# Kernel optimization log

Measured on AMD Instinct MI355X. Metric: run time of the kernel, lower is better.

The kernel has to match this reference:

```python
import jax, jax.numpy as jnp
import numpy as np

B, S, H, D = 2, 2048, 32, 128
DM = H * D  # 4096
SCALE = D ** -0.5


def setup_inputs() -> dict:
    key = jax.random.key(0)
    ks = jax.random.split(key, 7)
    std = DM ** -0.5
    return {
        "q": jax.random.normal(ks[0], (B, S, DM), dtype=jnp.float32),
        "k": jax.random.normal(ks[1], (B, S, DM), dtype=jnp.float32),
        "v": jax.random.normal(ks[2], (B, S, DM), dtype=jnp.float32),
        # torch nn.Linear weights are [out_features, in_features]
        "Wq": jax.random.normal(ks[3], (DM, DM), dtype=jnp.float32) * std,
        "Wk": jax.random.normal(ks[4], (DM, DM), dtype=jnp.float32) * std,
        "Wv": jax.random.normal(ks[5], (DM, DM), dtype=jnp.float32) * std,
        "Wo": jax.random.normal(ks[6], (DM, DM), dtype=jnp.float32) * std,
    }


def reference(q, k, v, Wq, Wk, Wv, Wo):
    # Linear: y = x @ W^T (no bias, qkv_bias=False)
    qp = q @ Wq.T  # [B,S,DM]
    kp = k @ Wk.T
    vp = v @ Wv.T
    # [B,S,DM] -> [B,H,S,D]
    qh = qp.reshape(B, S, H, D).transpose(0, 2, 1, 3)
    kh = kp.reshape(B, S, H, D).transpose(0, 2, 1, 3)
    vh = vp.reshape(B, S, H, D).transpose(0, 2, 1, 3)
    # scaled dot-product attention (no mask; attn_mask default None)
    scores = jnp.einsum("bhqd,bhkd->bhqk", qh, kh) * SCALE  # [B,H,S,S]
    probs = jax.nn.softmax(scores, axis=-1)
    ctx = jnp.einsum("bhqk,bhkd->bhqd", probs, vh)  # [B,H,S,D]
    ctx = ctx.transpose(0, 2, 1, 3).reshape(B, S, DM)
    return ctx @ Wo.T  # [B,S,DM]
```

## Files before the change

### kernel.cpp

```cpp
#include <hip/hip_runtime.h>
#include <hip/hip_bf16.h>
#include <stdint.h>


using u16 = unsigned short;
using u32 = unsigned int;

typedef __attribute__((ext_vector_type(8))) short bf16x8;
typedef __attribute__((ext_vector_type(8))) u16 u16x8;
typedef __attribute__((ext_vector_type(4))) float f32x4;

#define MFMA_BF16(A, B, C) __builtin_amdgcn_mfma_f32_16x16x32_bf16((A), (B), (C), 0, 0, 0)

static constexpr int kS = 2048, kDM = 4096, kD = 128;
static constexpr size_t kMat = (size_t)4096 * 4096;
static constexpr float kScaleLog2e = 0.08838834764831845f * 1.44269504088896340736f;

static __device__ __forceinline__ void gload_lds16(const u16* g, u16* l) {
  __builtin_amdgcn_global_load_lds((const __attribute__((address_space(1))) void*)g,
                                   (__attribute__((address_space(3))) void*)l, 16, 0, 0);
}

static __device__ __forceinline__ u16 f2bf(float f) {
  u32 u = __float_as_uint(f);
  u32 r = u + 0x7FFFu + ((u >> 16) & 1u);
  return (u16)(r >> 16);
}

static __device__ __forceinline__ float bf2f(u16 x) {
  return __uint_as_float((u32)x << 16);
}

static __device__ __forceinline__ u16 nbf(float f) {
  union { __hip_bfloat16 h; u16 u; } cv;
  cv.h = __float2bfloat16(f);
  return cv.u;
}

static __device__ __forceinline__ u16x8 cvt8(float4 a, float4 b) {
  u16x8 r;
  r[0] = f2bf(a.x); r[1] = f2bf(a.y); r[2] = f2bf(a.z); r[3] = f2bf(a.w);
  r[4] = f2bf(b.x); r[5] = f2bf(b.y); r[6] = f2bf(b.z); r[7] = f2bf(b.w);
  return r;
}

__global__ __launch_bounds__(256) void cvt_kernel(
    const float* __restrict__ s0, const float* __restrict__ s1,
    const float* __restrict__ s2, const float* __restrict__ s3,
    const float* __restrict__ s4, const float* __restrict__ s5,
    const float* __restrict__ s6, u16* __restrict__ dst) {
  const int y = blockIdx.y;
  const float* s = (y == 0) ? s0 : (y == 1) ? s1 : (y == 2) ? s2 : (y == 3) ? s3
                  : (y == 4) ? s4 : (y == 5) ? s5 : s6;
  u16* d = dst + (size_t)y * kMat;
  const size_t nchunk = kMat / 8;
  const size_t step = (size_t)gridDim.x * 256;
  for (size_t c = (size_t)blockIdx.x * 256 + threadIdx.x; c < nchunk; c += step) {
    const float* p = s + c * 8;
    float4 a = *(const float4*)p;
    float4 b = *(const float4*)(p + 4);
    *(u16x8*)(d + c * 8) = cvt8(a, b);
  }
}

template <bool TRANS, bool OUT_F32>
static __device__ __forceinline__ void gemm256(const u16* __restrict__ X,
                                               const u16* __restrict__ W,
                                               void* __restrict__ Yv,
                                               u16* __restrict__ lds) {
  constexpr int NT = kDM / 64;
  const int tid = threadIdx.x;
  const int lane = tid & 63;
  const int w = tid >> 6;
  const int fr = lane & 15;
  const int fq = lane >> 4;
  const int wr = w >> 2;
  const int wc = w & 3;
  const int m0 = blockIdx.y * 256;
  const int n0 = blockIdx.x * 256;

  const int srow = tid >> 3;
  const int scol = ((tid & 7) ^ (srow & 7)) * 8;
  const u16* Xrow = X + (size_t)(m0 + srow) * kDM + scol;
  const u16* Wrow = W + (size_t)(n0 + srow) * kDM + scol;
  const int w512 = w * 512;

  const int rBb = wc * 64 + fr;
  const int rAb = wr * 128 + fr;
  const int swz = fr & 7;

  f32x4 acc[8][4] = {};

#define STAGE2(ROWP, qrow, k0, ldq)                                       \
  do {                                                                    \
    gload_lds16((ROWP) + (size_t)(qrow) * kDM + (k0), &lds[(ldq) + w512]); \
    gload_lds16((ROWP) + (size_t)((qrow) + 64) * kDM + (k0),              \
                &lds[(ldq) + 4096 + w512]);                               \
  } while (0)

  STAGE2(Wrow, 0, 0, 0);
  STAGE2(Wrow, 128, 0, 8192);
  STAGE2(Xrow, 0, 0, 16384);
  STAGE2(Xrow, 128, 0, 24576);
  STAGE2(Wrow, 0, 64, 32768);
  STAGE2(Wrow, 128, 64, 32768 + 8192);
  STAGE2(Xrow, 0, 64, 32768 + 16384);
  asm volatile("s_waitcnt vmcnt(6)" ::: "memory");
  __builtin_amdgcn_s_barrier();

  for (int t = 0; t < NT; ++t) {
    const int d = t & 1;
    const int Boff = d * 32768;
    const int Aoff = Boff + 16384;
    bf16x8 bfr[4][2], af[8][2];

#pragma unroll
    for (int nf = 0; nf < 4; ++nf)
#pragma unroll
      for (int ks = 0; ks < 2; ++ks)
        bfr[nf][ks] = *(const bf16x8*)&lds[Boff + (rBb + nf * 16) * 64 +
                                           (((ks * 4 + fq) ^ swz) * 8)];
#pragma unroll
    for (int mi = 0; mi < 4; ++mi)
#pragma unroll
      for (int ks = 0; ks < 2; ++ks)
        af[mi][ks] = *(const bf16x8*)&lds[Aoff + (rAb + mi * 16) * 64 +
                                          (((ks * 4 + fq) ^ swz) * 8)];
    if (t + 1 < NT) STAGE2(Xrow, 128, (t + 1) * 64, ((t + 1) & 1) * 32768 + 24576);
    __builtin_amdgcn_s_barrier();
    __builtin_amdgcn_s_setprio(1);
#pragma unroll
    for (int mi = 0; mi < 2; ++mi)
#pragma unroll
      for (int nf = 0; nf < 4; ++nf)
#pragma unroll
        for (int ks = 0; ks < 2; ++ks)
          acc[mi][nf] = TRANS ? MFMA_BF16(bfr[nf][ks], af[mi][ks], acc[mi][nf])
                              : MFMA_BF16(af[mi][ks], bfr[nf][ks], acc[mi][nf]);
    __builtin_amdgcn_s_setprio(0);
    __builtin_amdgcn_s_barrier();

#pragma unroll
    for (int mi = 4; mi < 6; ++mi)
#pragma unroll
      for (int ks = 0; ks < 2; ++ks)
        af[mi][ks] = *(const bf16x8*)&lds[Aoff + (rAb + mi * 16) * 64 +
                                          (((ks * 4 + fq) ^ swz) * 8)];
    if (t + 2 < NT) STAGE2(Wrow, 0, (t + 2) * 64, d * 32768 + 0);
    __builtin_amdgcn_s_barrier();
    __builtin_amdgcn_s_setprio(1);
#pragma unroll
    for (int mi = 2; mi < 4; ++mi)
#pragma unroll
      for (int nf = 0; nf < 4; ++nf)
#pragma unroll
        for (int ks = 0; ks < 2; ++ks)
          acc[mi][nf] = TRANS ? MFMA_BF16(bfr[nf][ks], af[mi][ks], acc[mi][nf])
                              : MFMA_BF16(af[mi][ks], bfr[nf][ks], acc[mi][nf]);
    __builtin_amdgcn_s_setprio(0);
    __builtin_amdgcn_s_barrier();

#pragma unroll
    for (int mi = 6; mi < 8; ++mi)
#pragma unroll
      for (int ks = 0; ks < 2; ++ks)
        af[mi][ks] = *(const bf16x8*)&lds[Aoff + (rAb + mi * 16) * 64 +
                                          (((ks * 4 + fq) ^ swz) * 8)];
    if (t + 2 < NT) STAGE2(Wrow, 128, (t + 2) * 64, d * 32768 + 8192);
    __builtin_amdgcn_s_barrier();
    __builtin_amdgcn_s_setprio(1);
#pragma unroll
    for (int mi = 4; mi < 6; ++mi)
#pragma unroll
      for (int nf = 0; nf < 4; ++nf)
#pragma unroll
        for (int ks = 0; ks < 2; ++ks)
          acc[mi][nf] = TRANS ? MFMA_BF16(bfr[nf][ks], af[mi][ks], acc[mi][nf])
                              : MFMA_BF16(af[mi][ks], bfr[nf][ks], acc[mi][nf]);
    __builtin_amdgcn_s_setprio(0);
    asm volatile("s_waitcnt lgkmcnt(0)" ::: "memory");
    __builtin_amdgcn_s_barrier();

    if (t + 2 < NT) STAGE2(Xrow, 0, (t + 2) * 64, d * 32768 + 16384);
    __builtin_amdgcn_s_barrier();
    __builtin_amdgcn_s_setprio(1);
#pragma unroll
    for (int mi = 6; mi < 8; ++mi)
#pragma unroll
      for (int nf = 0; nf < 4; ++nf)
#pragma unroll
        for (int ks = 0; ks < 2; ++ks)
          acc[mi][nf] = TRANS ? MFMA_BF16(bfr[nf][ks], af[mi][ks], acc[mi][nf])
                              : MFMA_BF16(af[mi][ks], bfr[nf][ks], acc[mi][nf]);
    __builtin_amdgcn_s_setprio(0);
    if (t + 2 < NT)
      asm volatile("s_waitcnt vmcnt(6)" ::: "memory");
    else
      asm volatile("s_waitcnt vmcnt(0)" ::: "memory");
    __builtin_amdgcn_s_barrier();
  }
#undef STAGE2

#pragma unroll
  for (int mi = 0; mi < 8; ++mi)
#pragma unroll
    for (int nf = 0; nf < 4; ++nf) {
      int row, col;
      if constexpr (TRANS) {
        row = n0 + wc * 64 + nf * 16 + fq * 4;
        col = m0 + wr * 128 + mi * 16 + fr;
      } else {
        row = m0 + wr * 128 + mi * 16 + fq * 4;
        col = n0 + wc * 64 + nf * 16 + fr;
      }
      if constexpr (OUT_F32) {
        float* yp = (float*)Yv + (size_t)row * kDM + col;
#pragma unroll
        for (int i = 0; i < 4; ++i) yp[(size_t)i * kDM] = acc[mi][nf][i];
      } else {
        u16* yp = (u16*)Yv + (size_t)row * kDM + col;
#pragma unroll
        for (int i = 0; i < 4; ++i) yp[(size_t)i * kDM] = f2bf(acc[mi][nf][i]);
      }
    }
}

__global__ __launch_bounds__(512, 2) void proj_qk256_kernel(const u16* __restrict__ wsb,
                                                            u16* __restrict__ qp,
                                                            u16* __restrict__ kp) {
  __shared__ u16 lds[65536];
  const int z = blockIdx.z;
  gemm256<false, false>(wsb + (size_t)z * kMat, wsb + (size_t)(3 + z) * kMat,
                        z ? kp : qp, lds);
}

__global__ __launch_bounds__(512, 2) void proj_vT256_kernel(const u16* __restrict__ wsb,
                                                            u16* __restrict__ vpT) {
  __shared__ u16 lds[65536];
  gemm256<true, false>(wsb + 2 * kMat, wsb + 5 * kMat, vpT, lds);
}

__global__ __launch_bounds__(512, 2) void out_proj256_kernel(const u16* __restrict__ ctx,
                                                             const u16* __restrict__ Wob,
                                                             float* __restrict__ out) {
  __shared__ u16 lds[65536];
  gemm256<false, true>(ctx, Wob, out, lds);
}

template <bool A_BF16, bool TRANS, bool OUT_F32>
static __device__ __forceinline__ void gemm_conv(const void* Xv, const float* Wf,
                                                 void* Yv, u16* __restrict__ Als,
                                                 u16* __restrict__ Bls) {
  constexpr int KD = 4096;
  const int tid = threadIdx.x;
  const int lane = tid & 63;
  const int w = tid >> 6;
  const int fr = lane & 15;
  const int fq = lane >> 4;
  const int m0 = blockIdx.y * 128;
  const int n0 = blockIdx.x * 128;

  const int r0 = tid >> 2, cc0 = (tid & 3) * 8;
  const int r1 = r0 + 64;
  const int sr = lane >> 2, sc = (lane & 3) * 8;
  const int u0 = w * 2, u1 = w * 2 + 1;

  const u16* Xb = (const u16*)Xv;
  const float* Xf = (const float*)Xv;

  const int wm = (w >> 1) * 64;
  const int wn = (w & 1) * 64;

  f32x4 acc[4][4] = {};

  for (int kt = 0; kt < KD / 32; ++kt) {
    const int ko = kt * 32;
    if constexpr (A_BF16) {
      gload_lds16(Xb + (size_t)(m0 + u0 * 16 + sr) * KD + ko + sc, &Als[u0 * 512]);
      gload_lds16(Xb + (size_t)(m0 + u1 * 16 + sr) * KD + ko + sc, &Als[u1 * 512]);
    } else {
      const float* p0 = Xf + (size_t)(m0 + r0) * KD + ko + cc0;
      const float* p1 = Xf + (size_t)(m0 + r1) * KD + ko + cc0;
      float4 a0 = *(const float4*)(p0);
      float4 a1 = *(const float4*)(p0 + 4);
      float4 a2 = *(const float4*)(p1);
      float4 a3 = *(const float4*)(p1 + 4);
      *(u16x8*)&Als[r0 * 32 + cc0] = cvt8(a0, a1);
      *(u16x8*)&Als[r1 * 32 + cc0] = cvt8(a2, a3);
    }
    {
      const float* p0 = Wf + (size_t)(n0 + r0) * KD + ko + cc0;
      const float* p1 = Wf + (size_t)(n0 + r1) * KD + ko + cc0;
      float4 b0 = *(const float4*)(p0);
      float4 b1 = *(const float4*)(p0 + 4);
      float4 b2 = *(const float4*)(p1);
      float4 b3 = *(const float4*)(p1 + 4);
      *(u16x8*)&Bls[r0 * 32 + cc0] = cvt8(b0, b1);
      *(u16x8*)&Bls[r1 * 32 + cc0] = cvt8(b2, b3);
    }
    __syncthreads();

    bf16x8 af[4], bfv[4];
#pragma unroll
    for (int i = 0; i < 4; ++i)
      af[i] = *(const bf16x8*)&Als[(wm + i * 16 + fr) * 32 + fq * 8];
#pragma unroll
    for (int i = 0; i < 4; ++i)
      bfv[i] = *(const bf16x8*)&Bls[(wn + i * 16 + fr) * 32 + fq * 8];
#pragma unroll
    for (int a = 0; a < 4; ++a)
#pragma unroll
      for (int bb = 0; bb < 4; ++bb) {
        if constexpr (TRANS)
          acc[a][bb] = MFMA_BF16(bfv[a], af[bb], acc[a][bb]);
        else
          acc[a][bb] = MFMA_BF16(af[a], bfv[bb], acc[a][bb]);
      }
    __syncthreads();
  }

#pragma unroll
  for (int a = 0; a < 4; ++a)
#pragma unroll
    for (int bb = 0; bb < 4; ++bb) {
      const int row = TRANS ? (n0 + wn + a * 16 + fq * 4) : (m0 + wm + a * 16 + fq * 4);
      const int col = TRANS ? (m0 + wm + bb * 16 + fr) : (n0 + wn + bb * 16 + fr);
      if constexpr (OUT_F32) {
        float* yp = (float*)Yv + (size_t)row * kDM + col;
#pragma unroll
        for (int i = 0; i < 4; ++i) yp[(size_t)i * kDM] = acc[a][bb][i];
      } else {
        u16* yp = (u16*)Yv + (size_t)row * kDM + col;
#pragma unroll
        for (int i = 0; i < 4; ++i) yp[(size_t)i * kDM] = f2bf(acc[a][bb][i]);
      }
    }
}

__global__ __launch_bounds__(256) void proj_qk_conv_kernel(
    const float* __restrict__ q, const float* __restrict__ k,
    const float* __restrict__ Wq, const float* __restrict__ Wk,
    u16* __restrict__ qp, u16* __restrict__ kp) {
  __shared__ u16 Als[128 * 32];
  __shared__ u16 Bls[128 * 32];
  const int z = blockIdx.z;
  gemm_conv<false, false, false>(z ? k : q, z ? Wk : Wq, z ? kp : qp, Als, Bls);
}

__global__ __launch_bounds__(256) void proj_vT_conv_kernel(
    const float* __restrict__ v, const float* __restrict__ Wv, u16* __restrict__ vpT) {
  __shared__ u16 Als[128 * 32];
  __shared__ u16 Bls[128 * 32];
  gemm_conv<false, true, false>(v, Wv, vpT, Als, Bls);
}

__global__ __launch_bounds__(256) void out_proj_conv_kernel(const u16* __restrict__ ctx,
                                                            const float* __restrict__ Wo,
                                                            float* __restrict__ out) {
  __shared__ u16 Als[128 * 32];
  __shared__ u16 Bls[128 * 32];
  gemm_conv<true, false, true>(ctx, Wo, out, Als, Bls);
}

__global__ __launch_bounds__(512) void attn_kernel(const u16* __restrict__ qp,
                                                   const u16* __restrict__ kp,
                                                   const u16* __restrict__ vpT,
                                                   u16* __restrict__ ctx) {
  constexpr int KB = 64;
  constexpr int NT = kS / KB;
  constexpr int PST = 72;
  constexpr float THR = 11.5f;

  __shared__ u16 Kls[KB * 128];
  __shared__ u16 Vt[kD * KB];
  __shared__ u16 Pls[8][2 * 16 * PST];

  const int tid = threadIdx.x, lane = tid & 63, w = tid >> 6;
  const int fr = lane & 15, fq = lane >> 4;

  const int wg = blockIdx.y * 8 + blockIdx.x;
  const int o = (wg & 7) * 64 + (wg >> 3);
  const int bh = o >> 3;
  const int b = bh >> 5, h = bh & 31;
  const int q0 = (o & 7) * 256;

  const u16* qbase = qp + ((size_t)b * kS) * kDM + h * kD;
  const u16* kbase = kp + ((size_t)b * kS) * kDM + h * kD;
  const u16* vtbase = vpT + (size_t)(h * kD) * kDM + b * kS;

  bf16x8 qf[2][4];
#pragma unroll
  for (int rb = 0; rb < 2; ++rb)
#pragma unroll
    for (int kc = 0; kc < 4; ++kc) {
      const u16x8 raw = *(const u16x8*)(qbase +
          (size_t)(q0 + w * 32 + rb * 16 + fr) * kDM + kc * 32 + fq * 8);
      bf16x8 s;
#pragma unroll
      for (int j = 0; j < 8; ++j) s[j] = (short)f2bf(bf2f(raw[j]) * kScaleLog2e);
      qf[rb][kc] = s;
    }

  f32x4 oacc[2][9] = {};
  float mrun[2][4];
#pragma unroll
  for (int rb = 0; rb < 2; ++rb)
#pragma unroll
    for (int i = 0; i < 4; ++i) mrun[rb][i] = -1e30f;

  bf16x8 ones;
#pragma unroll
  for (int j = 0; j < 8; ++j) ones[j] = (short)0x3F80;

  const int krl = lane >> 4, kdp = lane & 15;
  const int vdl = lane >> 3, vc = lane & 7;
  const int rk0 = (w * 2 + 0) * 4 + krl;
  const int rk1 = (w * 2 + 1) * 4 + krl;
  const int dv0 = (w * 2 + 0) * 8 + vdl;
  const int dv1 = (w * 2 + 1) * 8 + vdl;
  const u16* kg0 = kbase + (size_t)rk0 * kDM + kdp * 8;
  const u16* kg1 = kbase + (size_t)rk1 * kDM + kdp * 8;
  const u16* vg0 = vtbase + (size_t)dv0 * kDM + vc * 8;
  const u16* vg1 = vtbase + (size_t)dv1 * kDM + vc * 8;
  u16* kl0 = &Kls[rk0 * 128 + ((kdp ^ (rk0 & 7)) * 8)];
  u16* kl1 = &Kls[rk1 * 128 + ((kdp ^ (rk1 & 7)) * 8)];
  u16* vl0 = &Vt[dv0 * KB + ((vc ^ (dv0 & 7)) * 8)];
  u16* vl1 = &Vt[dv1 * KB + ((vc ^ (dv1 & 7)) * 8)];

  u16x8 kr0v, kr1v, vr0v, vr1v;
  kr0v = *(const u16x8*)kg0;
  kr1v = *(const u16x8*)kg1;
  vr0v = *(const u16x8*)vg0;
  vr1v = *(const u16x8*)vg1;
  *(u16x8*)kl0 = kr0v; *(u16x8*)kl1 = kr1v;
  *(u16x8*)vl0 = vr0v; *(u16x8*)vl1 = vr1v;
  __syncthreads();

  for (int kt = 0; kt < NT; ++kt) {
    if (kt + 1 < NT) {
      const size_t ko = (size_t)(kt + 1) * KB;
      kr0v = *(const u16x8*)(kg0 + ko * kDM);
      kr1v = *(const u16x8*)(kg1 + ko * kDM);
      vr0v = *(const u16x8*)(vg0 + ko);
      vr1v = *(const u16x8*)(vg1 + ko);
    }

    f32x4 sacc[2][4] = {};
#pragma unroll
    for (int cb = 0; cb < 4; ++cb) {
      const int n = cb * 16 + fr;
      bf16x8 kf[4];
#pragma unroll
      for (int kc = 0; kc < 4; ++kc) {
        const int d0 = kc * 4 + fq;
        kf[kc] = *(const bf16x8*)&Kls[n * 128 + (d0 ^ (n & 7)) * 8];
      }
      __builtin_amdgcn_s_setprio(1);
#pragma unroll
      for (int rb = 0; rb < 2; ++rb)
#pragma unroll
        for (int kc = 0; kc < 4; ++kc)
          sacc[rb][cb] = MFMA_BF16(qf[rb][kc], kf[kc], sacc[rb][cb]);
      __builtin_amdgcn_s_setprio(0);
    }

#pragma unroll
    for (int rb = 0; rb < 2; ++rb) {
      float mt[4];
#pragma unroll
      for (int i = 0; i < 4; ++i)
        mt[i] = fmaxf(fmaxf(sacc[rb][0][i], sacc[rb][1][i]),
                      fmaxf(sacc[rb][2][i], sacc[rb][3][i]));
#pragma unroll
      for (int off = 1; off < 16; off <<= 1)
#pragma unroll
        for (int i = 0; i < 4; ++i) mt[i] = fmaxf(mt[i], __shfl_xor(mt[i], off));

      const float grow = fmaxf(fmaxf(mt[0] - mrun[rb][0], mt[1] - mrun[rb][1]),
                               fmaxf(mt[2] - mrun[rb][2], mt[3] - mrun[rb][3]));
      if (__any(grow > THR)) {
        float scl[4];
#pragma unroll
        for (int i = 0; i < 4; ++i) {
          const float mnew = fmaxf(mrun[rb][i], mt[i]);
          scl[i] = exp2f(mrun[rb][i] - mnew);
          mrun[rb][i] = mnew;
        }
#pragma unroll
        for (int db = 0; db < 9; ++db)
#pragma unroll
          for (int i = 0; i < 4; ++i) oacc[rb][db][i] *= scl[i];
      }

#pragma unroll
      for (int cb = 0; cb < 4; ++cb)
#pragma unroll
        for (int i = 0; i < 4; ++i) {
          const float p = exp2f(sacc[rb][cb][i] - mrun[rb][i]);
          Pls[w][rb * (16 * PST) + (fq * 4 + i) * PST + cb * 16 + fr] = nbf(p);
        }
    }

    asm volatile("s_waitcnt lgkmcnt(0)" ::: "memory");

    bf16x8 pf[2][2];
#pragma unroll
    for (int rb = 0; rb < 2; ++rb)
#pragma unroll
      for (int kb = 0; kb < 2; ++kb)
        pf[rb][kb] = *(const bf16x8*)&Pls[w][rb * (16 * PST) + fr * PST + kb * 32 + fq * 8];
#pragma unroll
    for (int db = 0; db < 8; ++db) {
      const int d = db * 16 + fr;
      bf16x8 vf0 = *(const bf16x8*)&Vt[d * KB + ((fq ^ (d & 7)) << 3)];
      bf16x8 vf1 = *(const bf16x8*)&Vt[d * KB + (((4 + fq) ^ (d & 7)) << 3)];
      __builtin_amdgcn_s_setprio(1);
#pragma unroll
      for (int rb = 0; rb < 2; ++rb) {
        oacc[rb][db] = MFMA_BF16(pf[rb][0], vf0, oacc[rb][db]);
        oacc[rb][db] = MFMA_BF16(pf[rb][1], vf1, oacc[rb][db]);
      }
      __builtin_amdgcn_s_setprio(0);
    }
    __builtin_amdgcn_s_setprio(1);
#pragma unroll
    for (int rb = 0; rb < 2; ++rb) {
      oacc[rb][8] = MFMA_BF16(pf[rb][0], ones, oacc[rb][8]);
      oacc[rb][8] = MFMA_BF16(pf[rb][1], ones, oacc[rb][8]);
    }
    __builtin_amdgcn_s_setprio(0);

    __syncthreads();
    if (kt + 1 < NT) {
      *(u16x8*)kl0 = kr0v; *(u16x8*)kl1 = kr1v;
      *(u16x8*)vl0 = vr0v; *(u16x8*)vl1 = vr1v;
    }
    __syncthreads();
  }

  u16* cbase = ctx + ((size_t)b * kS) * kDM + h * kD;
#pragma unroll
  for (int rb = 0; rb < 2; ++rb) {
    float inv[4];
#pragma unroll
    for (int i = 0; i < 4; ++i) inv[i] = 1.0f / oacc[rb][8][i];
#pragma unroll
    for (int db = 0; db < 8; ++db)
#pragma unroll
      for (int i = 0; i < 4; ++i) {
        const int row = q0 + w * 32 + rb * 16 + fq * 4 + i;
        const int col = db * 16 + fr;
        cbase[(size_t)row * kDM + col] = nbf(oacc[rb][db][i] * inv[i]);
      }
  }
}

extern "C" void kernel_launch(void* const* d_in, const int* in_sizes, int n_in,
                              void* d_out, int out_size, void* d_ws, size_t ws_size,
                              hipStream_t stream) {
  const float* q = (const float*)d_in[0];
  const float* k = (const float*)d_in[1];
  const float* v = (const float*)d_in[2];
  const float* Wq = (const float*)d_in[3];
  const float* Wk = (const float*)d_in[4];
  const float* Wv = (const float*)d_in[5];
  const float* Wo = (const float*)d_in[6];
  float* out = (float*)d_out;

  const size_t needFast = 11 * kMat * sizeof(u16);

  if (ws_size >= needFast) {
    u16* wsb = (u16*)d_ws;
    u16* qp = wsb + 7 * kMat;
    u16* kp = wsb + 8 * kMat;
    u16* vpT = wsb + 9 * kMat;
    u16* ctx = wsb + 10 * kMat;

    cvt_kernel<<<dim3(1024, 7), 256, 0, stream>>>(q, k, v, Wq, Wk, Wv, Wo, wsb);
    proj_qk256_kernel<<<dim3(16, 16, 2), 512, 0, stream>>>(wsb, qp, kp);
    proj_vT256_kernel<<<dim3(16, 16), 512, 0, stream>>>(wsb, vpT);
    attn_kernel<<<dim3(8, 64), 512, 0, stream>>>(qp, kp, vpT, ctx);
    out_proj256_kernel<<<dim3(16, 16), 512, 0, stream>>>(ctx, wsb + 6 * kMat, out);
  } else {
    u16* qp = (u16*)d_ws;
    u16* kp = qp + kMat;
    u16* vpT = kp + kMat;
    u16* ctx = vpT + kMat;

    proj_qk_conv_kernel<<<dim3(32, 32, 2), 256, 0, stream>>>(q, k, Wq, Wk, qp, kp);
    proj_vT_conv_kernel<<<dim3(32, 32), 256, 0, stream>>>(v, Wv, vpT);
    attn_kernel<<<dim3(8, 64), 512, 0, stream>>>(qp, kp, vpT, ctx);
    out_proj_conv_kernel<<<dim3(32, 32, 1), 256, 0, stream>>>(ctx, Wo, out);
  }
}
```

Before: 775.4 us.

## Swizzle GEMM tiles across XCDs and transpose QK^T MFMA for per-lane row softmax

The three 256x256 projection GEMMs now remap their flat block id with an XCD-aware swizzle, so neighbouring output tiles that share operand rows land on the same XCD and can reuse its L2. In the attention kernel the QK^T MFMA operands are swapped, so each lane holds scores for a single query row. The row max then needs only two cross-lane shuffles instead of four rounds over four values, and P is written to LDS as packed 4-element vectors rather than scalar stores. The rescale factors still have to be broadcast back to the output-accumulator layout with shuffles, and the new P store pattern may change LDS bank conflicts.

Result: faster. 743.9 us (-4.1%).

```diff
diff --git a/kernel.cpp b/kernel.cpp
--- a/kernel.cpp
+++ b/kernel.cpp
@@ -8,6 +8,7 @@
 
 typedef __attribute__((ext_vector_type(8))) short bf16x8;
 typedef __attribute__((ext_vector_type(8))) u16 u16x8;
+typedef __attribute__((ext_vector_type(4))) u16 u16x4;
 typedef __attribute__((ext_vector_type(4))) float f32x4;
 
 #define MFMA_BF16(A, B, C) __builtin_amdgcn_mfma_f32_16x16x32_bf16((A), (B), (C), 0, 0, 0)
@@ -67,7 +68,8 @@
 static __device__ __forceinline__ void gemm256(const u16* __restrict__ X,
                                                const u16* __restrict__ W,
                                                void* __restrict__ Yv,
-                                               u16* __restrict__ lds) {
+                                               u16* __restrict__ lds,
+                                               int m0, int n0) {
   constexpr int NT = kDM / 64;
   const int tid = threadIdx.x;
   const int lane = tid & 63;
@@ -76,8 +78,6 @@
   const int fq = lane >> 4;
   const int wr = w >> 2;
   const int wc = w & 3;
-  const int m0 = blockIdx.y * 256;
-  const int n0 = blockIdx.x * 256;
 
   const int srow = tid >> 3;
   const int scol = ((tid & 7) ^ (srow & 7)) * 8;
@@ -225,26 +225,38 @@
     }
 }
 
+static __device__ __forceinline__ int xcd_swz(int id, int cpx) {
+  return (id & 7) * cpx + (id >> 3);
+}
+
 __global__ __launch_bounds__(512, 2) void proj_qk256_kernel(const u16* __restrict__ wsb,
                                                             u16* __restrict__ qp,
                                                             u16* __restrict__ kp) {
   __shared__ u16 lds[65536];
-  const int z = blockIdx.z;
+  const int id = blockIdx.z * 256 + blockIdx.y * 16 + blockIdx.x;
+  const int s = xcd_swz(id, 64);
+  const int z = s >> 8;
+  const int m0 = ((s >> 4) & 15) * 256, n0 = (s & 15) * 256;
   gemm256<false, false>(wsb + (size_t)z * kMat, wsb + (size_t)(3 + z) * kMat,
-                        z ? kp : qp, lds);
+                        z ? kp : qp, lds, m0, n0);
 }
 
 __global__ __launch_bounds__(512, 2) void proj_vT256_kernel(const u16* __restrict__ wsb,
                                                             u16* __restrict__ vpT) {
   __shared__ u16 lds[65536];
-  gemm256<true, false>(wsb + 2 * kMat, wsb + 5 * kMat, vpT, lds);
+  const int id = blockIdx.y * 16 + blockIdx.x;
+  const int s = xcd_swz(id, 32);
+  gemm256<true, false>(wsb + 2 * kMat, wsb + 5 * kMat, vpT, lds,
+                       (s >> 4) * 256, (s & 15) * 256);
 }
 
 __global__ __launch_bounds__(512, 2) void out_proj256_kernel(const u16* __restrict__ ctx,
                                                              const u16* __restrict__ Wob,
                                                              float* __restrict__ out) {
   __shared__ u16 lds[65536];
-  gemm256<false, true>(ctx, Wob, out, lds);
+  const int id = blockIdx.y * 16 + blockIdx.x;
+  const int s = xcd_swz(id, 32);
+  gemm256<false, true>(ctx, Wob, out, lds, (s >> 4) * 256, (s & 15) * 256);
 }
 
 template <bool A_BF16, bool TRANS, bool OUT_F32>
@@ -402,11 +414,7 @@
     }
 
   f32x4 oacc[2][9] = {};
-  float mrun[2][4];
-#pragma unroll
-  for (int rb = 0; rb < 2; ++rb)
-#pragma unroll
-    for (int i = 0; i < 4; ++i) mrun[rb][i] = -1e30f;
+  float mrun[2] = {-1e30f, -1e30f};
 
   bf16x8 ones;
 #pragma unroll
@@ -460,32 +468,27 @@
       for (int rb = 0; rb < 2; ++rb)
 #pragma unroll
         for (int kc = 0; kc < 4; ++kc)
-          sacc[rb][cb] = MFMA_BF16(qf[rb][kc], kf[kc], sacc[rb][cb]);
+          sacc[rb][cb] = MFMA_BF16(kf[kc], qf[rb][kc], sacc[rb][cb]);
       __builtin_amdgcn_s_setprio(0);
     }
 
 #pragma unroll
     for (int rb = 0; rb < 2; ++rb) {
-      float mt[4];
-#pragma unroll
-      for (int i = 0; i < 4; ++i)
-        mt[i] = fmaxf(fmaxf(sacc[rb][0][i], sacc[rb][1][i]),
-                      fmaxf(sacc[rb][2][i], sacc[rb][3][i]));
-#pragma unroll
-      for (int off = 1; off < 16; off <<= 1)
-#pragma unroll
-        for (int i = 0; i < 4; ++i) mt[i] = fmaxf(mt[i], __shfl_xor(mt[i], off));
-
-      const float grow = fmaxf(fmaxf(mt[0] - mrun[rb][0], mt[1] - mrun[rb][1]),
-                               fmaxf(mt[2] - mrun[rb][2], mt[3] - mrun[rb][3]));
-      if (__any(grow > THR)) {
+      float m = sacc[rb][0][0];
+#pragma unroll
+      for (int cb = 0; cb < 4; ++cb)
+#pragma unroll
+        for (int i = 0; i < 4; ++i) m = fmaxf(m, sacc[rb][cb][i]);
+      m = fmaxf(m, __shfl_xor(m, 16));
+      m = fmaxf(m, __shfl_xor(m, 32));
+
+      if (__any(m - mrun[rb] > THR)) {
+        const float mnew = fmaxf(mrun[rb], m);
+        const float sclS = exp2f(mrun[rb] - mnew);
+        mrun[rb] = mnew;
         float scl[4];
 #pragma unroll
-        for (int i = 0; i < 4; ++i) {
-          const float mnew = fmaxf(mrun[rb][i], mt[i]);
-          scl[i] = exp2f(mrun[rb][i] - mnew);
-          mrun[rb][i] = mnew;
-        }
+        for (int i = 0; i < 4; ++i) scl[i] = __shfl(sclS, fq * 4 + i);
 #pragma unroll
         for (int db = 0; db < 9; ++db)
 #pragma unroll
@@ -493,12 +496,13 @@
       }
 
 #pragma unroll
-      for (int cb = 0; cb < 4; ++cb)
-#pragma unroll
-        for (int i = 0; i < 4; ++i) {
-          const float p = exp2f(sacc[rb][cb][i] - mrun[rb][i]);
-          Pls[w][rb * (16 * PST) + (fq * 4 + i) * PST + cb * 16 + fr] = nbf(p);
-        }
+      for (int cb = 0; cb < 4; ++cb) {
+        u16x4 pk;
+#pragma unroll
+        for (int i = 0; i < 4; ++i)
+          pk[i] = nbf(exp2f(sacc[rb][cb][i] - mrun[rb]));
+        *(u16x4*)&Pls[w][rb * (16 * PST) + fr * PST + cb * 16 + fq * 4] = pk;
+      }
     }
 
     asm volatile("s_waitcnt lgkmcnt(0)" ::: "memory");
```
